# Performance work log

Measured on AMD Instinct MI355X. Metric: run time of the kernel, lower is better.

## Reference

```python
import jax, jax.numpy as jnp
import numpy as np

EPS = 1e-7  # keras.backend.epsilon()
ROUTINGS = 3

def squash(v, axis=-1):
    s2 = jnp.sum(jnp.square(v), axis=axis, keepdims=True)
    scale = s2 / (1.0 + s2) / jnp.sqrt(s2 + EPS)
    return scale * v

def setup_inputs() -> dict:
    key = jax.random.key(0)
    k1, k2 = jax.random.split(key)
    B, J, I = 128, 2048, 8   # batch, input_num_capsule, input_dim_capsule
    K, D = 32, 16            # num_capsule, dim_capsule
    x = jax.random.normal(k1, (B, J, I), dtype=jnp.float32)
    W = jax.random.normal(k2, (J, K, I, D), dtype=jnp.float32) * 0.05
    return {"x": x, "W": W}

def reference(x, W):
    B = x.shape[0]
    K = W.shape[1]
    J = x.shape[1]
    # inputs_hat: [B, K, J, D]
    inputs_hat = jnp.einsum('bji,jkio->bkjo', x, W)
    b = jnp.zeros((B, K, J), dtype=x.dtype)
    v = None
    for i in range(ROUTINGS):
        c = jax.nn.softmax(b, axis=1)               # softmax over output capsules
        s = jnp.einsum('bkl,bkld->bkd', c, inputs_hat)
        v = squash(s)                               # [B, K, D]
        if i < ROUTINGS - 1:
            b = b + jnp.einsum('bkd,bkld->bkl', v, inputs_hat)
    return v
```

## Files before the change

kernel.cpp:

```cpp
#include <hip/hip_runtime.h>
#include <math.h>


constexpr int Bn = 128;
constexpr int Jn = 2048;
constexpr int In = 8;
constexpr int Kn = 32;
constexpr int Dn = 16;
constexpr int KD = Kn * Dn;
constexpr int CELLS = Bn * KD;

constexpr int JT    = 32;
constexpr int NJB   = Jn / JT;
constexpr int WAVES = 4;
constexpr int BLOCK = WAVES * 64;
constexpr int BW    = 2;
constexpr int BGW   = WAVES * BW;
constexpr int NBB   = Bn / BGW;
constexpr int GRID_SWEEP = NBB * NJB;
constexpr int WSLICE = Kn * In * Dn;
constexpr int WBYTES = WSLICE * 4;

__device__ __forceinline__ void stage_w(const float* __restrict__ Wj,
                                        float* dstf, int tid)
{
#pragma unroll
    for (int c = 0; c < 4; ++c) {
        const int M = c * 4096 + tid * 16;
        const int G = M ^ (((M >> 9) & 7) << 4);
        __builtin_amdgcn_global_load_lds(
            (const __attribute__((address_space(1))) void*)((const char*)Wj + G),
            (__attribute__((address_space(3))) void*)((char*)dstf + M),
            16, 0, 0);
    }
}

template <int PHASE, bool ATOMIC>
__global__ __launch_bounds__(BLOCK, 4)
void sweep_kernel(const float* __restrict__ x, const float* __restrict__ W,
                  const float* __restrict__ vsum, float* __restrict__ sout)
{
    __shared__ float wlds[2 * WSLICE];

    const int jb    = blockIdx.x % NJB;
    const int b0    = (blockIdx.x / NJB) * BGW;
    const int tid   = threadIdx.x;
    const int wave  = tid >> 6;
    const int lane  = tid & 63;
    const int kk    = lane >> 1;
    const int dh    = lane & 1;
    const int bbase = b0 + wave * BW;
    const int kmask = (kk & 7) << 4;
    const int Lbase = kk * 512 + dh * 32;

    float vs[BW][8];
    if (PHASE != 0) {
#pragma unroll
        for (int bb = 0; bb < BW; ++bb) {
            const float* vp = vsum + ((size_t)(bbase + bb) * Kn + kk) * Dn + dh * 8;
            const float4 a  = *reinterpret_cast<const float4*>(vp);
            const float4 b4 = *reinterpret_cast<const float4*>(vp + 4);
            vs[bb][0] = a.x;  vs[bb][1] = a.y;  vs[bb][2] = a.z;  vs[bb][3] = a.w;
            vs[bb][4] = b4.x; vs[bb][5] = b4.y; vs[bb][6] = b4.z; vs[bb][7] = b4.w;
        }
    }

    float sacc[BW][8];
#pragma unroll
    for (int bb = 0; bb < BW; ++bb)
#pragma unroll
        for (int r = 0; r < 8; ++r) sacc[bb][r] = 0.f;

    const int j0 = jb * JT;
    stage_w(W + (size_t)j0 * WSLICE, wlds, tid);
    __syncthreads();

#pragma unroll 2
    for (int jj = 0; jj < JT; ++jj) {
        const int j   = j0 + jj;
        const int buf = jj & 1;

        if (jj + 1 < JT)
            stage_w(W + (size_t)(j + 1) * WSLICE, wlds + (buf ^ 1) * WSLICE, tid);

        float xv[BW][8];
#pragma unroll
        for (int bb = 0; bb < BW; ++bb) {
            const float* xp = x + ((size_t)(bbase + bb) * Jn + j) * In;
            const float4 xa = *reinterpret_cast<const float4*>(xp);
            const float4 xb = *reinterpret_cast<const float4*>(xp + 4);
            xv[bb][0] = xa.x; xv[bb][1] = xa.y; xv[bb][2] = xa.z; xv[bb][3] = xa.w;
            xv[bb][4] = xb.x; xv[bb][5] = xb.y; xv[bb][6] = xb.z; xv[bb][7] = xb.w;
        }

        float uh[BW][8];
#pragma unroll
        for (int bb = 0; bb < BW; ++bb)
#pragma unroll
            for (int r = 0; r < 8; ++r) uh[bb][r] = 0.f;

        const char* wb = (const char*)wlds + buf * WBYTES;
#pragma unroll
        for (int i = 0; i < In; ++i) {
            const int a0 = (Lbase + i * 64) ^ kmask;
            const float4 wa = *reinterpret_cast<const float4*>(wb + a0);
            const float4 wc = *reinterpret_cast<const float4*>(wb + (a0 ^ 16));
            const float w8[8] = {wa.x, wa.y, wa.z, wa.w, wc.x, wc.y, wc.z, wc.w};
#pragma unroll
            for (int bb = 0; bb < BW; ++bb)
#pragma unroll
                for (int r = 0; r < 8; ++r)
                    uh[bb][r] = fmaf(xv[bb][i], w8[r], uh[bb][r]);
        }

        if (PHASE == 0) {
#pragma unroll
            for (int bb = 0; bb < BW; ++bb)
#pragma unroll
                for (int r = 0; r < 8; ++r) sacc[bb][r] += uh[bb][r];
        } else {
#pragma unroll
            for (int bb = 0; bb < BW; ++bb) {
                float p = vs[bb][0] * uh[bb][0];
#pragma unroll
                for (int r = 1; r < 8; ++r) p = fmaf(vs[bb][r], uh[bb][r], p);
                p += __shfl_xor(p, 1);

                const float e = __expf(p);
                float ss = e;
#pragma unroll
                for (int mk = 2; mk <= 32; mk <<= 1)
                    ss += __shfl_xor(ss, mk);
#if __has_builtin(__builtin_amdgcn_rcpf)
                const float c = e * __builtin_amdgcn_rcpf(ss);
#else
                const float c = e / ss;
#endif
#pragma unroll
                for (int r = 0; r < 8; ++r)
                    sacc[bb][r] = fmaf(c, uh[bb][r], sacc[bb][r]);
            }
        }
        __syncthreads();
    }

#pragma unroll
    for (int bb = 0; bb < BW; ++bb) {
        const int b = bbase + bb;
        const size_t cell = ((size_t)b * Kn + kk) * Dn + dh * 8;
        if (ATOMIC) {
#pragma unroll
            for (int r = 0; r < 8; ++r)
                atomicAdd(sout + cell + r, sacc[bb][r]);
        } else {
            const float4 f0 = make_float4(sacc[bb][0], sacc[bb][1], sacc[bb][2], sacc[bb][3]);
            const float4 f1 = make_float4(sacc[bb][4], sacc[bb][5], sacc[bb][6], sacc[bb][7]);
            float* dst = sout + (size_t)jb * CELLS + cell;
            *reinterpret_cast<float4*>(dst)     = f0;
            *reinterpret_cast<float4*>(dst + 4) = f1;
        }
    }
}

template <int PHASE, bool ATOMIC>
__global__ __launch_bounds__(256)
void squash_kernel(float* __restrict__ sbuf, float* __restrict__ vsum,
                   float* __restrict__ outv)
{
    const int t = blockIdx.x * blockDim.x + threadIdx.x;
    const size_t c4 = (size_t)t * 4;

    float4 s;
    if (ATOMIC) {
        s = *reinterpret_cast<const float4*>(sbuf + c4);
        *reinterpret_cast<float4*>(sbuf + c4) = make_float4(0.f, 0.f, 0.f, 0.f);
    } else {
        s = make_float4(0.f, 0.f, 0.f, 0.f);
#pragma unroll 4
        for (int p = 0; p < NJB; ++p) {
            const float4 v = *reinterpret_cast<const float4*>(sbuf + (size_t)p * CELLS + c4);
            s.x += v.x; s.y += v.y; s.z += v.z; s.w += v.w;
        }
    }

    if (PHASE == 0) {
        const float sc = 1.f / 32.f;
        s.x *= sc; s.y *= sc; s.z *= sc; s.w *= sc;
    }

    float s2 = s.x * s.x + s.y * s.y + s.z * s.z + s.w * s.w;
    s2 += __shfl_xor(s2, 1);
    s2 += __shfl_xor(s2, 2);
    const float scale = s2 / ((1.f + s2) * sqrtf(s2 + 1e-7f));
    const float4 v4 = make_float4(s.x * scale, s.y * scale, s.z * scale, s.w * scale);

    if (PHASE == 2) {
        *reinterpret_cast<float4*>(outv + c4) = v4;
    } else if (PHASE == 0) {
        *reinterpret_cast<float4*>(vsum + c4) = v4;
    } else {
        float4 o = *reinterpret_cast<const float4*>(vsum + c4);
        o.x += v4.x; o.y += v4.y; o.z += v4.z; o.w += v4.w;
        *reinterpret_cast<float4*>(vsum + c4) = o;
    }
}

extern "C" void kernel_launch(void* const* d_in, const int* in_sizes, int n_in,
                              void* d_out, int out_size, void* d_ws, size_t ws_size,
                              hipStream_t stream)
{
    const float* x = (const float*)d_in[0];
    const float* W = (const float*)d_in[1];
    float* out = (float*)d_out;

    const size_t partial_bytes = (size_t)NJB * CELLS * sizeof(float);
    const size_t vsum_bytes    = (size_t)CELLS * sizeof(float);

    const dim3 gs(GRID_SWEEP), bs(BLOCK);
    const dim3 gq(CELLS / 4 / 256), bq(256);

    if (ws_size >= partial_bytes + vsum_bytes) {
        float* partial = (float*)d_ws;
        float* vsum    = (float*)((char*)d_ws + partial_bytes);
        sweep_kernel<0, false><<<gs, bs, 0, stream>>>(x, W, vsum, partial);
        squash_kernel<0, false><<<gq, bq, 0, stream>>>(partial, vsum, out);
        sweep_kernel<1, false><<<gs, bs, 0, stream>>>(x, W, vsum, partial);
        squash_kernel<1, false><<<gq, bq, 0, stream>>>(partial, vsum, out);
        sweep_kernel<2, false><<<gs, bs, 0, stream>>>(x, W, vsum, partial);
        squash_kernel<2, false><<<gq, bq, 0, stream>>>(partial, vsum, out);
    } else {
        float* sbuf = (float*)d_ws;
        float* vsum = (float*)((char*)d_ws + vsum_bytes);
        hipMemsetAsync(sbuf, 0, vsum_bytes, stream);
        sweep_kernel<0, true><<<gs, bs, 0, stream>>>(x, W, vsum, sbuf);
        squash_kernel<0, true><<<gq, bq, 0, stream>>>(sbuf, vsum, out);
        sweep_kernel<1, true><<<gs, bs, 0, stream>>>(x, W, vsum, sbuf);
        squash_kernel<1, true><<<gq, bq, 0, stream>>>(sbuf, vsum, out);
        sweep_kernel<2, true><<<gs, bs, 0, stream>>>(x, W, vsum, sbuf);
        squash_kernel<2, true><<<gq, bq, 0, stream>>>(sbuf, vsum, out);
    }
}
```

Baseline: 284.4 us.

## Stage W tiles in LDS as fp16 via register prefetch instead of direct loads

W slices are now loaded into registers one iteration ahead, converted to packed fp16, and written to swizzled LDS, replacing the direct global-to-LDS fp32 copies. This halves the LDS footprint and per-lane LDS read traffic (one 16-byte read per i instead of two) and could allow more resident blocks. In exchange it adds conversion ALU work, extra registers for the staged data, and reduced precision in W, which may shift results relative to the fp32 reference.

```diff
diff --git a/kernel.cpp b/kernel.cpp
--- a/kernel.cpp
+++ b/kernel.cpp
@@ -1,4 +1,5 @@
 #include <hip/hip_runtime.h>
+#include <hip/hip_fp16.h>
 #include <math.h>
 
 
@@ -18,21 +19,37 @@
 constexpr int BGW   = WAVES * BW;
 constexpr int NBB   = Bn / BGW;
 constexpr int GRID_SWEEP = NBB * NJB;
-constexpr int WSLICE = Kn * In * Dn;
-constexpr int WBYTES = WSLICE * 4;
-
-__device__ __forceinline__ void stage_w(const float* __restrict__ Wj,
-                                        float* dstf, int tid)
-{
-#pragma unroll
-    for (int c = 0; c < 4; ++c) {
-        const int M = c * 4096 + tid * 16;
-        const int G = M ^ (((M >> 9) & 7) << 4);
-        __builtin_amdgcn_global_load_lds(
-            (const __attribute__((address_space(1))) void*)((const char*)Wj + G),
-            (__attribute__((address_space(3))) void*)((char*)dstf + M),
-            16, 0, 0);
-    }
+constexpr int SLICE = Kn * In * Dn * 2;
+
+__device__ __forceinline__ int swz(int L) { return L ^ (((L >> 8) & 7) << 4); }
+
+__device__ __forceinline__ unsigned pk2(float a, float b) {
+    const __half2 h = __floats2half2_rn(a, b);
+    return *reinterpret_cast<const unsigned*>(&h);
+}
+
+__device__ __forceinline__ void issue_loads(const float* __restrict__ W,
+                                            int jidx, int tid, float4 (&st)[4])
+{
+    const float* p = W + (size_t)jidx * 4096 + tid * 8;
+    st[0] = *reinterpret_cast<const float4*>(p);
+    st[1] = *reinterpret_cast<const float4*>(p + 4);
+    st[2] = *reinterpret_cast<const float4*>(p + 2048);
+    st[3] = *reinterpret_cast<const float4*>(p + 2052);
+}
+
+__device__ __forceinline__ void write_stage(char* ldsbase, int tid,
+                                            const float4 (&st)[4])
+{
+    uint4 u0, u1;
+    u0.x = pk2(st[0].x, st[0].y); u0.y = pk2(st[0].z, st[0].w);
+    u0.z = pk2(st[1].x, st[1].y); u0.w = pk2(st[1].z, st[1].w);
+    u1.x = pk2(st[2].x, st[2].y); u1.y = pk2(st[2].z, st[2].w);
+    u1.z = pk2(st[3].x, st[3].y); u1.w = pk2(st[3].z, st[3].w);
+    const int L0 = tid * 16;
+    const int L1 = tid * 16 + 4096;
+    *reinterpret_cast<uint4*>(ldsbase + swz(L0)) = u0;
+    *reinterpret_cast<uint4*>(ldsbase + swz(L1)) = u1;
 }
 
 template <int PHASE, bool ATOMIC>
@@ -40,7 +57,7 @@
 void sweep_kernel(const float* __restrict__ x, const float* __restrict__ W,
                   const float* __restrict__ vsum, float* __restrict__ sout)
 {
-    __shared__ float wlds[2 * WSLICE];
+    __shared__ __align__(16) char wlds[2 * SLICE];
 
     const int jb    = blockIdx.x % NJB;
     const int b0    = (blockIdx.x / NJB) * BGW;
@@ -50,8 +67,8 @@
     const int kk    = lane >> 1;
     const int dh    = lane & 1;
     const int bbase = b0 + wave * BW;
-    const int kmask = (kk & 7) << 4;
-    const int Lbase = kk * 512 + dh * 32;
+    const int kswz  = (kk & 7) << 4;
+    const int Lb    = kk * 256 + dh * 16;
 
     float vs[BW][8];
     if (PHASE != 0) {
@@ -72,16 +89,16 @@
         for (int r = 0; r < 8; ++r) sacc[bb][r] = 0.f;
 
     const int j0 = jb * JT;
-    stage_w(W + (size_t)j0 * WSLICE, wlds, tid);
+    float4 st[4];
+    issue_loads(W, j0, tid, st);
+    write_stage(wlds, tid, st);
+    issue_loads(W, j0 + 1, tid, st);
     __syncthreads();
 
 #pragma unroll 2
     for (int jj = 0; jj < JT; ++jj) {
         const int j   = j0 + jj;
         const int buf = jj & 1;
-
-        if (jj + 1 < JT)
-            stage_w(W + (size_t)(j + 1) * WSLICE, wlds + (buf ^ 1) * WSLICE, tid);
 
         float xv[BW][8];
 #pragma unroll
@@ -99,13 +116,21 @@
 #pragma unroll
             for (int r = 0; r < 8; ++r) uh[bb][r] = 0.f;
 
-        const char* wb = (const char*)wlds + buf * WBYTES;
+        const char* wb = wlds + buf * SLICE;
 #pragma unroll
         for (int i = 0; i < In; ++i) {
-            const int a0 = (Lbase + i * 64) ^ kmask;
-            const float4 wa = *reinterpret_cast<const float4*>(wb + a0);
-            const float4 wc = *reinterpret_cast<const float4*>(wb + (a0 ^ 16));
-            const float w8[8] = {wa.x, wa.y, wa.z, wa.w, wc.x, wc.y, wc.z, wc.w};
+            const uint4 wv = *reinterpret_cast<const uint4*>(wb + ((Lb + i * 32) ^ kswz));
+            float w8[8];
+            {
+                const __half2 h0 = *reinterpret_cast<const __half2*>(&wv.x);
+                const __half2 h1 = *reinterpret_cast<const __half2*>(&wv.y);
+                const __half2 h2 = *reinterpret_cast<const __half2*>(&wv.z);
+                const __half2 h3 = *reinterpret_cast<const __half2*>(&wv.w);
+                w8[0] = __low2float(h0); w8[1] = __high2float(h0);
+                w8[2] = __low2float(h1); w8[3] = __high2float(h1);
+                w8[4] = __low2float(h2); w8[5] = __high2float(h2);
+                w8[6] = __low2float(h3); w8[7] = __high2float(h3);
+            }
 #pragma unroll
             for (int bb = 0; bb < BW; ++bb)
 #pragma unroll
@@ -140,6 +165,11 @@
                 for (int r = 0; r < 8; ++r)
                     sacc[bb][r] = fmaf(c, uh[bb][r], sacc[bb][r]);
             }
+        }
+
+        if (jj + 1 < JT) {
+            write_stage(wlds + (buf ^ 1) * SLICE, tid, st);
+            if (jj + 2 < JT) issue_loads(W, j0 + jj + 2, tid, st);
         }
         __syncthreads();
     }
```

After: 1.103 ms. 3.88x slower.
